# Performance work log

Measured on AMD Instinct MI355X. Metric: run time of the kernel, lower is better.

Reference implementation:

```python
import jax, jax.numpy as jnp
import numpy as np

N = 100000
E = 2000000
F = 64          # in_features == out_features (required by attention * h_j)
BETA = 0.5
NEG_SLOPE = 0.01  # torch F.leaky_relu default


def setup_inputs() -> dict:
    key = jax.random.key(0)
    k1, k2, k3, k4, k5, k6 = jax.random.split(key, 6)
    h = jax.random.normal(k1, (N, F), dtype=jnp.float32)
    adj = jax.random.randint(k2, (2, E), 0, N, dtype=jnp.int64)
    amount = jax.random.uniform(k3, (E,), dtype=jnp.float32)
    count = jax.random.uniform(k4, (E,), dtype=jnp.float32)
    fc_w = jax.random.normal(k5, (F, 2 * F), dtype=jnp.float32) * (1.0 / np.sqrt(2 * F))
    fc_b = jax.random.normal(k6, (F,), dtype=jnp.float32) * 0.01
    return {"h": h, "adj": adj, "amount": amount, "count": count,
            "fc_w": fc_w, "fc_b": fc_b}


def _minmax_norm(x):
    lo, hi = x.min(), x.max()
    return (x - lo) / (hi - lo + 1e-8)


def reference(h, adj, amount, count, fc_w, fc_b):
    # per-edge weight from normalized amount/count
    edge_weight = BETA * _minmax_norm(amount) + (1.0 - BETA) * _minmax_norm(count)  # [E]

    src, dst = adj[0], adj[1]
    h_i = h[src]                     # [E, F]
    h_j = h[dst]                     # [E, F]
    h_cat = jnp.concatenate([h_i, h_j], axis=1)  # [E, 2F]

    score = jnp.einsum('ef,of->eo', h_cat, fc_w) + fc_b  # [E, F_out]
    score = jnp.where(score >= 0, score, NEG_SLOPE * score)  # leaky_relu
    score = score * edge_weight[:, None]

    # softmax over ALL edges (dim 0), per feature, as in the original
    attention = jax.nn.softmax(score, axis=0)  # [E, F]

    agg = jnp.zeros_like(h).at[src].add(attention * h_j)  # scatter-add -> [N, F]
    return agg
```

## Files before the change

### kernel.cpp

```cpp
#include <hip/hip_runtime.h>
#include <hip/hip_fp16.h>
#include <math.h>

#define FDIM   64
#define NB     64
#define BSHIFT 9
#define BMASK  511
#define EPTA   16
#define CHUNKA (EPTA * 256)
#define SCH    1024
#define DMASK  0xFFFFF

__global__ __launch_bounds__(256) void count_mm_k(const int* __restrict__ src,
                                                  const float* __restrict__ amount,
                                                  const float* __restrict__ count,
                                                  int* __restrict__ mat,
                                                  float4* __restrict__ partial,
                                                  double* __restrict__ colsum,
                                                  int E, int nblkA, int nbkt) {
  __shared__ int lhist[512];
  __shared__ float4 lred[4];
  for (int k = threadIdx.x; k < nbkt; k += 256) lhist[k] = 0;
  if (blockIdx.x == 0)
    for (int i = threadIdx.x; i < 1024; i += 256) colsum[i] = 0.0;
  __syncthreads();
  float amin = 3.4e38f, amax = -3.4e38f, cmin = 3.4e38f, cmax = -3.4e38f;
  int e0 = blockIdx.x * CHUNKA + threadIdx.x * EPTA;
  if (e0 + EPTA <= E) {
    #pragma unroll
    for (int q = 0; q < EPTA; q += 4) {
      int4   s4 = *(const int4*)(src + e0 + q);
      float4 a4 = *(const float4*)(amount + e0 + q);
      float4 c4 = *(const float4*)(count + e0 + q);
      atomicAdd(&lhist[s4.x >> BSHIFT], 1);
      atomicAdd(&lhist[s4.y >> BSHIFT], 1);
      atomicAdd(&lhist[s4.z >> BSHIFT], 1);
      atomicAdd(&lhist[s4.w >> BSHIFT], 1);
      amin = fminf(amin, fminf(fminf(a4.x, a4.y), fminf(a4.z, a4.w)));
      amax = fmaxf(amax, fmaxf(fmaxf(a4.x, a4.y), fmaxf(a4.z, a4.w)));
      cmin = fminf(cmin, fminf(fminf(c4.x, c4.y), fminf(c4.z, c4.w)));
      cmax = fmaxf(cmax, fmaxf(fmaxf(c4.x, c4.y), fmaxf(c4.z, c4.w)));
    }
  } else {
    for (int e = e0; e < E; e++) {
      atomicAdd(&lhist[src[e] >> BSHIFT], 1);
      float a = amount[e], c = count[e];
      amin = fminf(amin, a); amax = fmaxf(amax, a);
      cmin = fminf(cmin, c); cmax = fmaxf(cmax, c);
    }
  }
  #pragma unroll
  for (int off = 32; off; off >>= 1) {
    amin = fminf(amin, __shfl_down(amin, off));
    amax = fmaxf(amax, __shfl_down(amax, off));
    cmin = fminf(cmin, __shfl_down(cmin, off));
    cmax = fmaxf(cmax, __shfl_down(cmax, off));
  }
  if ((threadIdx.x & 63) == 0) lred[threadIdx.x >> 6] = make_float4(amin, amax, cmin, cmax);
  __syncthreads();
  for (int k = threadIdx.x; k < nbkt; k += 256)
    mat[(size_t)k * nblkA + blockIdx.x] = lhist[k];
  if (threadIdx.x == 0) {
    float4 r = lred[0];
    #pragma unroll
    for (int w = 1; w < 4; w++) {
      r.x = fminf(r.x, lred[w].x); r.y = fmaxf(r.y, lred[w].y);
      r.z = fminf(r.z, lred[w].z); r.w = fmaxf(r.w, lred[w].w);
    }
    partial[blockIdx.x] = r;
  }
}

__global__ __launch_bounds__(256) void scan1_k(const int* __restrict__ v,
                                               int* __restrict__ bsum, int M) {
  __shared__ int lds[256];
  int t = threadIdx.x, b = blockIdx.x;
  int s = 0;
  for (int i = b * SCH + t; i < min((b + 1) * SCH, M); i += 256) s += v[i];
  lds[t] = s; __syncthreads();
  for (int off = 128; off; off >>= 1) {
    if (t < off) lds[t] += lds[t + off];
    __syncthreads();
  }
  if (t == 0) bsum[b] = lds[0];
}

__global__ __launch_bounds__(256) void scan2_k(const int* __restrict__ bsum,
                                               int* __restrict__ bexcl, int nchunk,
                                               const float4* __restrict__ partial,
                                               float* __restrict__ mmf, int nb) {
  __shared__ int lds[256];
  int t = threadIdx.x;
  int running = 0;
  for (int c0 = 0; c0 < nchunk; c0 += 256) {
    int x = (c0 + t < nchunk) ? bsum[c0 + t] : 0;
    lds[t] = x; __syncthreads();
    for (int off = 1; off < 256; off <<= 1) {
      int v = (t >= off) ? lds[t - off] : 0;
      __syncthreads();
      lds[t] += v; __syncthreads();
    }
    if (c0 + t < nchunk) bexcl[c0 + t] = running + lds[t] - x;
    running += lds[255];
    __syncthreads();
  }
  float amin = 3.4e38f, amax = -3.4e38f, cmin = 3.4e38f, cmax = -3.4e38f;
  for (int i = t; i < nb; i += 256) {
    float4 p = partial[i];
    amin = fminf(amin, p.x); amax = fmaxf(amax, p.y);
    cmin = fminf(cmin, p.z); cmax = fmaxf(cmax, p.w);
  }
  #pragma unroll
  for (int off = 32; off; off >>= 1) {
    amin = fminf(amin, __shfl_down(amin, off));
    amax = fmaxf(amax, __shfl_down(amax, off));
    cmin = fminf(cmin, __shfl_down(cmin, off));
    cmax = fmaxf(cmax, __shfl_down(cmax, off));
  }
  __shared__ float4 lred[4];
  if ((t & 63) == 0) lred[t >> 6] = make_float4(amin, amax, cmin, cmax);
  __syncthreads();
  if (t == 0) {
    float4 r = lred[0];
    #pragma unroll
    for (int w = 1; w < 4; w++) {
      r.x = fminf(r.x, lred[w].x); r.y = fmaxf(r.y, lred[w].y);
      r.z = fminf(r.z, lred[w].z); r.w = fmaxf(r.w, lred[w].w);
    }
    mmf[0] = r.x; mmf[1] = r.y; mmf[2] = r.z; mmf[3] = r.w;
  }
}

__global__ __launch_bounds__(256) void scan3_k(const int* __restrict__ v,
                                               const int* __restrict__ bexcl,
                                               int* __restrict__ smat, int M) {
  __shared__ int lds[256];
  int t = threadIdx.x, b = blockIdx.x;
  int running = bexcl[b];
  for (int tile = 0; tile < SCH; tile += 256) {
    int i = b * SCH + tile + t;
    int x = (i < M) ? v[i] : 0;
    lds[t] = x; __syncthreads();
    for (int off = 1; off < 256; off <<= 1) {
      int vv = (t >= off) ? lds[t - off] : 0;
      __syncthreads();
      lds[t] += vv; __syncthreads();
    }
    if (i < M) smat[i] = running + lds[t] - x;
    running += lds[255];
    __syncthreads();
  }
}

__global__ __launch_bounds__(256) void scatter_k(const int* __restrict__ src,
                                                 const int* __restrict__ dst,
                                                 const float* __restrict__ amount,
                                                 const float* __restrict__ count,
                                                 const float* __restrict__ mmf,
                                                 const int* __restrict__ smat,
                                                 int2* __restrict__ payload,
                                                 int E, int nblkA, int nbkt) {
  __shared__ int cntb[512];
  __shared__ int baseb[512];
  __shared__ int sbase[512];
  __shared__ int wsum[4];
  __shared__ int2 lpay[CHUNKA];
  __shared__ int lgpos[CHUNKA];
  const int t = threadIdx.x, blk = blockIdx.x;
  for (int k = t; k < nbkt; k += 256) {
    cntb[k] = 0;
    sbase[k] = smat[(size_t)k * nblkA + blk];
  }
  __syncthreads();
  const float amin = mmf[0], amax = mmf[1], cmin = mmf[2], cmax = mmf[3];
  const float L2E = 1.4426950408889634f;
  const float ascale = 0.5f * L2E / (amax - amin + 1e-8f);
  const float cscale = 0.5f * L2E / (cmax - cmin + 1e-8f);
  int e0 = blk * CHUNKA + t * EPTA;
  const bool full = (e0 + EPTA <= E);
  int4 S[4]; int4 D[4]; float4 A[4]; float4 C[4];
  if (full) {
    #pragma unroll
    for (int q = 0; q < 4; q++) {
      S[q] = *(const int4*)(src + e0 + 4 * q);
      D[q] = *(const int4*)(dst + e0 + 4 * q);
      A[q] = *(const float4*)(amount + e0 + 4 * q);
      C[q] = *(const float4*)(count + e0 + 4 * q);
      atomicAdd(&cntb[S[q].x >> BSHIFT], 1);
      atomicAdd(&cntb[S[q].y >> BSHIFT], 1);
      atomicAdd(&cntb[S[q].z >> BSHIFT], 1);
      atomicAdd(&cntb[S[q].w >> BSHIFT], 1);
    }
  } else {
    for (int e = e0; e < E; e++) atomicAdd(&cntb[src[e] >> BSHIFT], 1);
  }
  __syncthreads();
  {
    const int wv = t >> 6, ln = t & 63;
    int carry = 0;
    #pragma unroll
    for (int c = 0; c < 4; c++) {
      int idx = (wv << 8) + (c << 6) + ln;
      int x = (idx < nbkt) ? cntb[idx] : 0;
      int v = x;
      #pragma unroll
      for (int off = 1; off < 64; off <<= 1) {
        int u = __shfl_up(v, off);
        if (ln >= off) v += u;
      }
      if (idx < nbkt) baseb[idx] = carry + v - x;
      carry += __shfl(v, 63);
    }
    if (ln == 0) wsum[wv] = carry;
  }
  __syncthreads();
  {
    const int wv = t >> 6, ln = t & 63;
    int wpre = 0;
    #pragma unroll
    for (int i = 0; i < 4; i++) wpre += (i < wv) ? wsum[i] : 0;
    if (wpre) {
      #pragma unroll
      for (int c = 0; c < 4; c++) {
        int idx = (wv << 8) + (c << 6) + ln;
        if (idx < nbkt) baseb[idx] += wpre;
      }
    }
  }
  __syncthreads();
  for (int k = t; k < nbkt; k += 256) cntb[k] = baseb[k];
  __syncthreads();
  auto ins = [&](int s, int d, float a, float c) {
    int b = s >> BSHIFT;
    float ew = (a - amin) * ascale + (c - cmin) * cscale;
    int pos = atomicAdd(&cntb[b], 1);
    lpay[pos] = make_int2(d | ((s & BMASK) << 20), __float_as_int(ew));
    lgpos[pos] = sbase[b] + (pos - baseb[b]);
  };
  if (full) {
    #pragma unroll
    for (int q = 0; q < 4; q++) {
      ins(S[q].x, D[q].x, A[q].x, C[q].x);
      ins(S[q].y, D[q].y, A[q].y, C[q].y);
      ins(S[q].z, D[q].z, A[q].z, C[q].z);
      ins(S[q].w, D[q].w, A[q].w, C[q].w);
    }
  } else {
    for (int e = e0; e < E; e++) ins(src[e], dst[e], amount[e], count[e]);
  }
  __syncthreads();
  const int ned = min(CHUNKA, E - blk * CHUNKA);
  for (int i = t; i < ned; i += 256) payload[lgpos[i]] = lpay[i];
}

__global__ __launch_bounds__(256) void binB_k(const int2* __restrict__ payload,
                                              const int* __restrict__ smat,
                                              int2* __restrict__ edge_s,
                                              int E, int nblkA, int nbkt) {
  __shared__ int fcnt[512];
  __shared__ int fbase[512];
  __shared__ int tmp[256];
  const int b = blockIdx.x;
  const int t = threadIdx.x;
  const int base = smat[(size_t)b * nblkA];
  const int end  = (b + 1 < nbkt) ? smat[(size_t)(b + 1) * nblkA] : E;
  fcnt[t] = 0; fcnt[t + 256] = 0;
  __syncthreads();
  for (int i = base + t; i < end; i += 256)
    atomicAdd(&fcnt[payload[i].x >> 20], 1);
  __syncthreads();
  int running = 0;
  for (int c0 = 0; c0 < 512; c0 += 256) {
    int x = fcnt[c0 + t];
    tmp[t] = x; __syncthreads();
    for (int off = 1; off < 256; off <<= 1) {
      int v = (t >= off) ? tmp[t - off] : 0;
      __syncthreads();
      tmp[t] += v; __syncthreads();
    }
    fbase[c0 + t] = running + tmp[t] - x;
    running += tmp[255];
    __syncthreads();
  }
  fcnt[t] = base + fbase[t];
  fcnt[t + 256] = base + fbase[t + 256];
  __syncthreads();
  for (int i = base + t; i < end; i += 256) {
    int2 v = payload[i];
    int pos = atomicAdd(&fcnt[v.x >> 20], 1);
    edge_s[pos] = v;
  }
}

__global__ __launch_bounds__(128) void pre_gemm(const float* __restrict__ h,
                                                const float* __restrict__ fc_w,
                                                const float* __restrict__ fc_b,
                                                float* __restrict__ G1,
                                                __half2* __restrict__ P, int N) {
  __shared__ float hs[NB * FDIM];
  const int t = threadIdx.x;
  const int o = t & 63, half = t >> 6;
  float w[FDIM];
  const float* wrow = fc_w + o * 128 + half * 64;
  #pragma unroll
  for (int f = 0; f < FDIM; f += 4) {
    float4 v = *(const float4*)(wrow + f);
    w[f] = v.x; w[f + 1] = v.y; w[f + 2] = v.z; w[f + 3] = v.w;
  }
  const float bias = (half == 0) ? fc_b[o] : 0.0f;
  const int n0 = blockIdx.x * NB;
  const int nrows = min(NB, N - n0);
  {
    const float4* hsrc = (const float4*)(h + (size_t)n0 * FDIM);
    float4* hd = (float4*)hs;
    for (int i = t; i < nrows * (FDIM / 4); i += 128) hd[i] = hsrc[i];
  }
  __syncthreads();
  for (int n = 0; n < nrows; n++) {
    float acc = bias;
    #pragma unroll
    for (int f = 0; f < FDIM; f += 4) {
      float4 hv = *(const float4*)(&hs[n * FDIM + f]);
      acc += hv.x * w[f] + hv.y * w[f + 1] + hv.z * w[f + 2] + hv.w * w[f + 3];
    }
    if (half == 0) {
      G1[(size_t)(n0 + n) * FDIM + o] = acc;
    } else {
      P[(size_t)(n0 + n) * FDIM + o] =
          __halves2half2(__float2half(acc), __float2half(hs[n * FDIM + o]));
    }
  }
}

__device__ __forceinline__ float2 unpack_h2(unsigned u) {
  __half2 v = *(__half2*)&u;
  return make_float2(__low2float(v), __high2float(v));
}

__global__ __launch_bounds__(256) void fused_k(const int2* __restrict__ edge_s,
                                               const int* __restrict__ smat,
                                               const float* __restrict__ G1,
                                               const unsigned* __restrict__ P,
                                               double* __restrict__ colsum,
                                               float* __restrict__ out,
                                               int E, int nblkA, int nbkt) {
  const int lane = threadIdx.x & 63;
  const int wv = __builtin_amdgcn_readfirstlane(threadIdx.x >> 6);
  const int wid = blockIdx.x * 4 + wv;
  const int nw = gridDim.x * 4;
  float csum = 0.0f;
  const int per = (((E + nw - 1) / nw) + 63) & ~63;
  const int e0 = wid * per;
  const int e1 = min(e0 + per, E);
  if (e0 < E) {
    int lo = 0, hi = nbkt - 1;
    while (lo < hi) {
      int mid = (lo + hi + 1) >> 1;
      if (smat[(size_t)mid * nblkA] <= e0) lo = mid; else hi = mid - 1;
    }
    int bkt = lo;
    int nextb = (bkt + 1 < nbkt) ? smat[(size_t)(bkt + 1) * nblkA] : E;
    int curnode = -1;
    bool firstf = true;
    float acc = 0.0f, g1 = 0.0f;
    auto flush_to = [&](int node) {
      if (curnode >= 0) {
        float* dp = out + (size_t)curnode * FDIM + lane;
        if (firstf) { atomicAdd(dp, acc); firstf = false; }
        else *dp = acc;
      }
      curnode = node; acc = 0.0f;
      g1 = G1[(size_t)node * FDIM + lane];
    };
    for (int c0 = e0; c0 < e1; c0 += 64) {
      const int m = min(64, e1 - c0);
      int2 p = make_int2(0, 0);
      if (lane < m) p = edge_s[c0 + lane];
      if (m == 64) {
        #pragma unroll 1
        for (int j = 0; j < 64; j += 16) {
          int dd[16], nd[16]; float ee[16]; unsigned uu[16];
          #pragma unroll
          for (int k = 0; k < 16; k++) {
            int x = __builtin_amdgcn_readlane(p.x, j + k);
            ee[k] = __int_as_float(__builtin_amdgcn_readlane(p.y, j + k));
            dd[k] = x & DMASK;
            nd[k] = x >> 20;
          }
          #pragma unroll
          for (int k = 0; k < 16; k++) uu[k] = P[(size_t)dd[k] * FDIM + lane];
          #pragma unroll
          for (int k = 0; k < 16; k++) {
            int i = c0 + j + k;
            while (i >= nextb) { bkt++; nextb = (bkt + 1 < nbkt) ? smat[(size_t)(bkt + 1) * nblkA] : E; }
            int node = (bkt << BSHIFT) + nd[k];
            if (node != curnode) flush_to(node);
            float2 v = unpack_h2(uu[k]);
            float sc = g1 + v.x;
            sc = fmaxf(sc, 0.01f * sc);
            float x = exp2f(sc * ee[k]);
            csum += x;
            acc += x * v.y;
          }
        }
      } else {
        for (int j = 0; j < m; j += 16) {
          const int rem = m - j;
          int dd[16], nd[16]; float ee[16]; unsigned uu[16];
          #pragma unroll
          for (int k = 0; k < 16; k++) {
            int x = __builtin_amdgcn_readlane(p.x, j + k);
            ee[k] = __int_as_float(__builtin_amdgcn_readlane(p.y, j + k));
            dd[k] = x & DMASK;
            nd[k] = x >> 20;
          }
          #pragma unroll
          for (int k = 0; k < 16; k++) uu[k] = P[(size_t)dd[k] * FDIM + lane];
          #pragma unroll
          for (int k = 0; k < 16; k++) {
            if (k < rem) {
              int i = c0 + j + k;
              while (i >= nextb) { bkt++; nextb = (bkt + 1 < nbkt) ? smat[(size_t)(bkt + 1) * nblkA] : E; }
              int node = (bkt << BSHIFT) + nd[k];
              if (node != curnode) flush_to(node);
              float2 v = unpack_h2(uu[k]);
              float sc = g1 + v.x;
              sc = fmaxf(sc, 0.01f * sc);
              float x = exp2f(sc * ee[k]);
              csum += x;
              acc += x * v.y;
            }
          }
        }
      }
    }
    if (curnode >= 0) atomicAdd(out + (size_t)curnode * FDIM + lane, acc);
  }
  __shared__ float part[256];
  part[threadIdx.x] = csum;
  __syncthreads();
  if (threadIdx.x < 64) {
    float tot = part[threadIdx.x] + part[threadIdx.x + 64] +
                part[threadIdx.x + 128] + part[threadIdx.x + 192];
    atomicAdd(&colsum[threadIdx.x * 16], (double)tot);
  }
}

__global__ __launch_bounds__(256) void scale_k(float4* __restrict__ out4,
                                               const double* __restrict__ colsum,
                                               int total4) {
  __shared__ float rinv_s[64];
  if (threadIdx.x < 64) rinv_s[threadIdx.x] = (float)(1.0 / colsum[threadIdx.x * 16]);
  __syncthreads();
  const float4* r4 = (const float4*)rinv_s;
  int idx = blockIdx.x * blockDim.x + threadIdx.x;
  int stride = gridDim.x * blockDim.x;
  for (int i = idx; i < total4; i += stride) {
    float4 v = out4[i];
    float4 r = r4[i & 15];
    v.x *= r.x; v.y *= r.y; v.z *= r.z; v.w *= r.w;
    out4[i] = v;
  }
}

extern "C" void kernel_launch(void* const* d_in, const int* in_sizes, int n_in,
                              void* d_out, int out_size, void* d_ws, size_t ws_size,
                              hipStream_t stream) {
  const float* h      = (const float*)d_in[0];
  const int*   adj    = (const int*)d_in[1];
  const float* amount = (const float*)d_in[2];
  const float* count  = (const float*)d_in[3];
  const float* fc_w   = (const float*)d_in[4];
  const float* fc_b   = (const float*)d_in[5];
  float* out = (float*)d_out;

  const int E = in_sizes[2];
  const int N = in_sizes[0] / FDIM;
  const int* src = adj;
  const int* dst = adj + E;
  const int nbkt  = (N + BMASK) >> BSHIFT;
  const int nblkA = (E + CHUNKA - 1) / CHUNKA;
  const int M = nbkt * nblkA;
  const int nchunk = (M + SCH - 1) / SCH;

  char* ws = (char*)d_ws;
  size_t off = 0;
  auto alloc = [&](size_t bytes) { void* p = ws + off; off += (bytes + 255) & ~(size_t)255; return p; };
  float*    G1      = (float*)alloc((size_t)N * FDIM * sizeof(float));
  __half2*  P       = (__half2*)alloc((size_t)N * FDIM * sizeof(__half2));
  int2*     edge_s  = (int2*)alloc((size_t)E * sizeof(int2));
  int2*     payload = (int2*)alloc((size_t)E * sizeof(int2));
  int*      mat     = (int*)alloc((size_t)M * sizeof(int));
  int*      smat    = (int*)alloc((size_t)M * sizeof(int));
  int*      bsum    = (int*)alloc((size_t)nchunk * sizeof(int));
  int*      bexcl   = (int*)alloc((size_t)nchunk * sizeof(int));
  float4*   mmpart  = (float4*)alloc((size_t)nblkA * sizeof(float4));
  double*   colsum  = (double*)alloc(1024 * sizeof(double));
  float*    mmf     = (float*)alloc(4 * sizeof(float));

  hipMemsetAsync(d_out, 0, (size_t)out_size * sizeof(float), stream);
  count_mm_k<<<nblkA, 256, 0, stream>>>(src, amount, count, mat, mmpart, colsum, E, nblkA, nbkt);
  scan1_k<<<nchunk, 256, 0, stream>>>(mat, bsum, M);
  scan2_k<<<1, 256, 0, stream>>>(bsum, bexcl, nchunk, mmpart, mmf, nblkA);
  scan3_k<<<nchunk, 256, 0, stream>>>(mat, bexcl, smat, M);
  scatter_k<<<nblkA, 256, 0, stream>>>(src, dst, amount, count, mmf, smat, payload, E, nblkA, nbkt);
  binB_k<<<nbkt, 256, 0, stream>>>(payload, smat, edge_s, E, nblkA, nbkt);
  pre_gemm<<<(N + NB - 1) / NB, 128, 0, stream>>>(h, fc_w, fc_b, G1, P, N);
  fused_k<<<4096, 256, 0, stream>>>(edge_s, smat, G1, (const unsigned*)P, colsum, out, E, nblkA, nbkt);
  scale_k<<<1024, 256, 0, stream>>>((float4*)out, colsum, N * FDIM / 4);
}
```

Baseline: 307.2 us.

## Replace per-block histogram matrix scans with global atomic bucket cursors

Measured after the change: 314.2 us. 2.3% more time.

```diff
diff --git a/kernel.cpp b/kernel.cpp
--- a/kernel.cpp
+++ b/kernel.cpp
@@ -3,26 +3,23 @@
 #include <math.h>
 
 #define FDIM   64
-#define NB     64
-#define BSHIFT 9
-#define BMASK  511
+#define NB     128
+#define BSHIFT 8
+#define BMASK  255
 #define EPTA   16
 #define CHUNKA (EPTA * 256)
-#define SCH    1024
 #define DMASK  0xFFFFF
+#define MAXBKT 512
 
 __global__ __launch_bounds__(256) void count_mm_k(const int* __restrict__ src,
                                                   const float* __restrict__ amount,
                                                   const float* __restrict__ count,
-                                                  int* __restrict__ mat,
+                                                  int* __restrict__ bktTotal,
                                                   float4* __restrict__ partial,
-                                                  double* __restrict__ colsum,
-                                                  int E, int nblkA, int nbkt) {
-  __shared__ int lhist[512];
+                                                  int E, int nbkt) {
+  __shared__ int lhist[MAXBKT];
   __shared__ float4 lred[4];
   for (int k = threadIdx.x; k < nbkt; k += 256) lhist[k] = 0;
-  if (blockIdx.x == 0)
-    for (int i = threadIdx.x; i < 1024; i += 256) colsum[i] = 0.0;
   __syncthreads();
   float amin = 3.4e38f, amax = -3.4e38f, cmin = 3.4e38f, cmax = -3.4e38f;
   int e0 = blockIdx.x * CHUNKA + threadIdx.x * EPTA;
@@ -59,7 +56,7 @@
   if ((threadIdx.x & 63) == 0) lred[threadIdx.x >> 6] = make_float4(amin, amax, cmin, cmax);
   __syncthreads();
   for (int k = threadIdx.x; k < nbkt; k += 256)
-    mat[(size_t)k * nblkA + blockIdx.x] = lhist[k];
+    if (lhist[k]) atomicAdd(&bktTotal[k], lhist[k]);
   if (threadIdx.x == 0) {
     float4 r = lred[0];
     #pragma unroll
@@ -71,39 +68,35 @@
   }
 }
 
-__global__ __launch_bounds__(256) void scan1_k(const int* __restrict__ v,
-                                               int* __restrict__ bsum, int M) {
-  __shared__ int lds[256];
-  int t = threadIdx.x, b = blockIdx.x;
-  int s = 0;
-  for (int i = b * SCH + t; i < min((b + 1) * SCH, M); i += 256) s += v[i];
-  lds[t] = s; __syncthreads();
-  for (int off = 128; off; off >>= 1) {
-    if (t < off) lds[t] += lds[t + off];
+__global__ __launch_bounds__(256) void scanB_k(const int* __restrict__ bktTotal,
+                                               int* __restrict__ bbase,
+                                               int* __restrict__ cursor,
+                                               const float4* __restrict__ partial,
+                                               float* __restrict__ mmf,
+                                               int nbkt, int nb, int E) {
+  __shared__ int lds[MAXBKT];
+  const int t = threadIdx.x;
+  for (int k = t; k < nbkt; k += 256) lds[k] = bktTotal[k];
+  __syncthreads();
+  __shared__ int tmp[256];
+  int running = 0;
+  for (int c0 = 0; c0 < nbkt; c0 += 256) {
+    int x = (c0 + t < nbkt) ? lds[c0 + t] : 0;
+    tmp[t] = x; __syncthreads();
+    for (int off = 1; off < 256; off <<= 1) {
+      int v = (t >= off) ? tmp[t - off] : 0;
+      __syncthreads();
+      tmp[t] += v; __syncthreads();
+    }
+    if (c0 + t < nbkt) {
+      int b = running + tmp[t] - x;
+      bbase[c0 + t] = b;
+      cursor[c0 + t] = b;
+    }
+    running += tmp[255];
     __syncthreads();
   }
-  if (t == 0) bsum[b] = lds[0];
-}
-
-__global__ __launch_bounds__(256) void scan2_k(const int* __restrict__ bsum,
-                                               int* __restrict__ bexcl, int nchunk,
-                                               const float4* __restrict__ partial,
-                                               float* __restrict__ mmf, int nb) {
-  __shared__ int lds[256];
-  int t = threadIdx.x;
-  int running = 0;
-  for (int c0 = 0; c0 < nchunk; c0 += 256) {
-    int x = (c0 + t < nchunk) ? bsum[c0 + t] : 0;
-    lds[t] = x; __syncthreads();
-    for (int off = 1; off < 256; off <<= 1) {
-      int v = (t >= off) ? lds[t - off] : 0;
-      __syncthreads();
-      lds[t] += v; __syncthreads();
-    }
-    if (c0 + t < nchunk) bexcl[c0 + t] = running + lds[t] - x;
-    running += lds[255];
-    __syncthreads();
-  }
+  if (t == 0) bbase[nbkt] = E;
   float amin = 3.4e38f, amax = -3.4e38f, cmin = 3.4e38f, cmax = -3.4e38f;
   for (int i = t; i < nb; i += 256) {
     float4 p = partial[i];
@@ -131,52 +124,24 @@
   }
 }
 
-__global__ __launch_bounds__(256) void scan3_k(const int* __restrict__ v,
-                                               const int* __restrict__ bexcl,
-                                               int* __restrict__ smat, int M) {
-  __shared__ int lds[256];
-  int t = threadIdx.x, b = blockIdx.x;
-  int running = bexcl[b];
-  for (int tile = 0; tile < SCH; tile += 256) {
-    int i = b * SCH + tile + t;
-    int x = (i < M) ? v[i] : 0;
-    lds[t] = x; __syncthreads();
-    for (int off = 1; off < 256; off <<= 1) {
-      int vv = (t >= off) ? lds[t - off] : 0;
-      __syncthreads();
-      lds[t] += vv; __syncthreads();
-    }
-    if (i < M) smat[i] = running + lds[t] - x;
-    running += lds[255];
-    __syncthreads();
-  }
-}
-
 __global__ __launch_bounds__(256) void scatter_k(const int* __restrict__ src,
                                                  const int* __restrict__ dst,
                                                  const float* __restrict__ amount,
                                                  const float* __restrict__ count,
                                                  const float* __restrict__ mmf,
-                                                 const int* __restrict__ smat,
+                                                 int* __restrict__ cursor,
                                                  int2* __restrict__ payload,
-                                                 int E, int nblkA, int nbkt) {
-  __shared__ int cntb[512];
-  __shared__ int baseb[512];
-  __shared__ int sbase[512];
-  __shared__ int wsum[4];
-  __shared__ int2 lpay[CHUNKA];
-  __shared__ int lgpos[CHUNKA];
-  const int t = threadIdx.x, blk = blockIdx.x;
-  for (int k = t; k < nbkt; k += 256) {
-    cntb[k] = 0;
-    sbase[k] = smat[(size_t)k * nblkA + blk];
-  }
+                                                 int E, int nbkt) {
+  __shared__ int lhist[MAXBKT];
+  __shared__ int lcur[MAXBKT];
+  const int t = threadIdx.x;
+  for (int k = t; k < nbkt; k += 256) lhist[k] = 0;
   __syncthreads();
   const float amin = mmf[0], amax = mmf[1], cmin = mmf[2], cmax = mmf[3];
   const float L2E = 1.4426950408889634f;
   const float ascale = 0.5f * L2E / (amax - amin + 1e-8f);
   const float cscale = 0.5f * L2E / (cmax - cmin + 1e-8f);
-  int e0 = blk * CHUNKA + t * EPTA;
+  int e0 = blockIdx.x * CHUNKA + t * EPTA;
   const bool full = (e0 + EPTA <= E);
   int4 S[4]; int4 D[4]; float4 A[4]; float4 C[4];
   if (full) {
@@ -186,56 +151,23 @@
       D[q] = *(const int4*)(dst + e0 + 4 * q);
       A[q] = *(const float4*)(amount + e0 + 4 * q);
       C[q] = *(const float4*)(count + e0 + 4 * q);
-      atomicAdd(&cntb[S[q].x >> BSHIFT], 1);
-      atomicAdd(&cntb[S[q].y >> BSHIFT], 1);
-      atomicAdd(&cntb[S[q].z >> BSHIFT], 1);
-      atomicAdd(&cntb[S[q].w >> BSHIFT], 1);
+      atomicAdd(&lhist[S[q].x >> BSHIFT], 1);
+      atomicAdd(&lhist[S[q].y >> BSHIFT], 1);
+      atomicAdd(&lhist[S[q].z >> BSHIFT], 1);
+      atomicAdd(&lhist[S[q].w >> BSHIFT], 1);
     }
   } else {
-    for (int e = e0; e < E; e++) atomicAdd(&cntb[src[e] >> BSHIFT], 1);
-  }
-  __syncthreads();
-  {
-    const int wv = t >> 6, ln = t & 63;
-    int carry = 0;
-    #pragma unroll
-    for (int c = 0; c < 4; c++) {
-      int idx = (wv << 8) + (c << 6) + ln;
-      int x = (idx < nbkt) ? cntb[idx] : 0;
-      int v = x;
-      #pragma unroll
-      for (int off = 1; off < 64; off <<= 1) {
-        int u = __shfl_up(v, off);
-        if (ln >= off) v += u;
-      }
-      if (idx < nbkt) baseb[idx] = carry + v - x;
-      carry += __shfl(v, 63);
-    }
-    if (ln == 0) wsum[wv] = carry;
-  }
-  __syncthreads();
-  {
-    const int wv = t >> 6, ln = t & 63;
-    int wpre = 0;
-    #pragma unroll
-    for (int i = 0; i < 4; i++) wpre += (i < wv) ? wsum[i] : 0;
-    if (wpre) {
-      #pragma unroll
-      for (int c = 0; c < 4; c++) {
-        int idx = (wv << 8) + (c << 6) + ln;
-        if (idx < nbkt) baseb[idx] += wpre;
-      }
-    }
-  }
-  __syncthreads();
-  for (int k = t; k < nbkt; k += 256) cntb[k] = baseb[k];
+    for (int e = e0; e < E; e++) atomicAdd(&lhist[src[e] >> BSHIFT], 1);
+  }
+  __syncthreads();
+  for (int k = t; k < nbkt; k += 256)
+    lcur[k] = lhist[k] ? atomicAdd(&cursor[k], lhist[k]) : 0;
   __syncthreads();
   auto ins = [&](int s, int d, float a, float c) {
     int b = s >> BSHIFT;
     float ew = (a - amin) * ascale + (c - cmin) * cscale;
-    int pos = atomicAdd(&cntb[b], 1);
-    lpay[pos] = make_int2(d | ((s & BMASK) << 20), __float_as_int(ew));
-    lgpos[pos] = sbase[b] + (pos - baseb[b]);
+    int pos = atomicAdd(&lcur[b], 1);
+    payload[pos] = make_int2(d | ((s & BMASK) << 20), __float_as_int(ew));
   };
   if (full) {
     #pragma unroll
@@ -248,58 +180,48 @@
   } else {
     for (int e = e0; e < E; e++) ins(src[e], dst[e], amount[e], count[e]);
   }
-  __syncthreads();
-  const int ned = min(CHUNKA, E - blk * CHUNKA);
-  for (int i = t; i < ned; i += 256) payload[lgpos[i]] = lpay[i];
 }
 
 __global__ __launch_bounds__(256) void binB_k(const int2* __restrict__ payload,
-                                              const int* __restrict__ smat,
+                                              const int* __restrict__ bbase,
                                               int2* __restrict__ edge_s,
-                                              int E, int nblkA, int nbkt) {
-  __shared__ int fcnt[512];
-  __shared__ int fbase[512];
+                                              int E, int nbkt) {
+  __shared__ int fcnt[256];
   __shared__ int tmp[256];
+  __shared__ int fcur[256];
   const int b = blockIdx.x;
   const int t = threadIdx.x;
-  const int base = smat[(size_t)b * nblkA];
-  const int end  = (b + 1 < nbkt) ? smat[(size_t)(b + 1) * nblkA] : E;
-  fcnt[t] = 0; fcnt[t + 256] = 0;
+  const int base = bbase[b];
+  const int end  = bbase[b + 1];
+  fcnt[t] = 0;
   __syncthreads();
   for (int i = base + t; i < end; i += 256)
-    atomicAdd(&fcnt[payload[i].x >> 20], 1);
-  __syncthreads();
-  int running = 0;
-  for (int c0 = 0; c0 < 512; c0 += 256) {
-    int x = fcnt[c0 + t];
-    tmp[t] = x; __syncthreads();
-    for (int off = 1; off < 256; off <<= 1) {
-      int v = (t >= off) ? tmp[t - off] : 0;
-      __syncthreads();
-      tmp[t] += v; __syncthreads();
-    }
-    fbase[c0 + t] = running + tmp[t] - x;
-    running += tmp[255];
+    atomicAdd(&fcnt[(payload[i].x >> 20) & BMASK], 1);
+  __syncthreads();
+  int x = fcnt[t];
+  tmp[t] = x; __syncthreads();
+  for (int off = 1; off < 256; off <<= 1) {
+    int v = (t >= off) ? tmp[t - off] : 0;
     __syncthreads();
-  }
-  fcnt[t] = base + fbase[t];
-  fcnt[t + 256] = base + fbase[t + 256];
+    tmp[t] += v; __syncthreads();
+  }
+  fcur[t] = base + tmp[t] - x;
   __syncthreads();
   for (int i = base + t; i < end; i += 256) {
     int2 v = payload[i];
-    int pos = atomicAdd(&fcnt[v.x >> 20], 1);
+    int pos = atomicAdd(&fcur[(v.x >> 20) & BMASK], 1);
     edge_s[pos] = v;
   }
 }
 
-__global__ __launch_bounds__(128) void pre_gemm(const float* __restrict__ h,
+__global__ __launch_bounds__(256) void pre_gemm(const float* __restrict__ h,
                                                 const float* __restrict__ fc_w,
                                                 const float* __restrict__ fc_b,
                                                 float* __restrict__ G1,
                                                 __half2* __restrict__ P, int N) {
   __shared__ float hs[NB * FDIM];
   const int t = threadIdx.x;
-  const int o = t & 63, half = t >> 6;
+  const int o = t & 63, half = (t >> 6) & 1, rg = t >> 7;
   float w[FDIM];
   const float* wrow = fc_w + o * 128 + half * 64;
   #pragma unroll
@@ -313,10 +235,12 @@
   {
     const float4* hsrc = (const float4*)(h + (size_t)n0 * FDIM);
     float4* hd = (float4*)hs;
-    for (int i = t; i < nrows * (FDIM / 4); i += 128) hd[i] = hsrc[i];
-  }
-  __syncthreads();
-  for (int n = 0; n < nrows; n++) {
+    for (int i = t; i < nrows * (FDIM / 4); i += 256) hd[i] = hsrc[i];
+  }
+  __syncthreads();
+  const int r0 = rg * 64;
+  const int r1 = min(r0 + 64, nrows);
+  for (int n = r0; n < r1; n++) {
     float acc = bias;
     #pragma unroll
     for (int f = 0; f < FDIM; f += 4) {
@@ -338,12 +262,12 @@
 }
 
 __global__ __launch_bounds__(256) void fused_k(const int2* __restrict__ edge_s,
-                                               const int* __restrict__ smat,
+                                               const int* __restrict__ bbase,
                                                const float* __restrict__ G1,
                                                const unsigned* __restrict__ P,
                                                double* __restrict__ colsum,
                                                float* __restrict__ out,
-                                               int E, int nblkA, int nbkt) {
+                                               int E, int nbkt) {
   const int lane = threadIdx.x & 63;
   const int wv = __builtin_amdgcn_readfirstlane(threadIdx.x >> 6);
   const int wid = blockIdx.x * 4 + wv;
@@ -356,10 +280,10 @@
     int lo = 0, hi = nbkt - 1;
     while (lo < hi) {
       int mid = (lo + hi + 1) >> 1;
-      if (smat[(size_t)mid * nblkA] <= e0) lo = mid; else hi = mid - 1;
+      if (bbase[mid] <= e0) lo = mid; else hi = mid - 1;
     }
     int bkt = lo;
-    int nextb = (bkt + 1 < nbkt) ? smat[(size_t)(bkt + 1) * nblkA] : E;
+    int nextb = bbase[bkt + 1];
     int curnode = -1;
     bool firstf = true;
     float acc = 0.0f, g1 = 0.0f;
@@ -385,14 +309,14 @@
             int x = __builtin_amdgcn_readlane(p.x, j + k);
             ee[k] = __int_as_float(__builtin_amdgcn_readlane(p.y, j + k));
             dd[k] = x & DMASK;
-            nd[k] = x >> 20;
+            nd[k] = (x >> 20) & BMASK;
           }
           #pragma unroll
           for (int k = 0; k < 16; k++) uu[k] = P[(size_t)dd[k] * FDIM + lane];
           #pragma unroll
           for (int k = 0; k < 16; k++) {
             int i = c0 + j + k;
-            while (i >= nextb) { bkt++; nextb = (bkt + 1 < nbkt) ? smat[(size_t)(bkt + 1) * nblkA] : E; }
+            while (i >= nextb) { bkt++; nextb = bbase[bkt + 1]; }
             int node = (bkt << BSHIFT) + nd[k];
             if (node != curnode) flush_to(node);
             float2 v = unpack_h2(uu[k]);
@@ -412,7 +336,7 @@
             int x = __builtin_amdgcn_readlane(p.x, j + k);
             ee[k] = __int_as_float(__builtin_amdgcn_readlane(p.y, j + k));
             dd[k] = x & DMASK;
-            nd[k] = x >> 20;
+            nd[k] = (x >> 20) & BMASK;
           }
           #pragma unroll
           for (int k = 0; k < 16; k++) uu[k] = P[(size_t)dd[k] * FDIM + lane];
@@ -420,7 +344,7 @@
           for (int k = 0; k < 16; k++) {
             if (k < rem) {
               int i = c0 + j + k;
-              while (i >= nextb) { bkt++; nextb = (bkt + 1 < nbkt) ? smat[(size_t)(bkt + 1) * nblkA] : E; }
+              while (i >= nextb) { bkt++; nextb = bbase[bkt + 1]; }
               int node = (bkt << BSHIFT) + nd[k];
               if (node != curnode) flush_to(node);
               float2 v = unpack_h2(uu[k]);
@@ -480,32 +404,29 @@
   const int* dst = adj + E;
   const int nbkt  = (N + BMASK) >> BSHIFT;
   const int nblkA = (E + CHUNKA - 1) / CHUNKA;
-  const int M = nbkt * nblkA;
-  const int nchunk = (M + SCH - 1) / SCH;
 
   char* ws = (char*)d_ws;
   size_t off = 0;
   auto alloc = [&](size_t bytes) { void* p = ws + off; off += (bytes + 255) & ~(size_t)255; return p; };
-  float*    G1      = (float*)alloc((size_t)N * FDIM * sizeof(float));
-  __half2*  P       = (__half2*)alloc((size_t)N * FDIM * sizeof(__half2));
-  int2*     edge_s  = (int2*)alloc((size_t)E * sizeof(int2));
-  int2*     payload = (int2*)alloc((size_t)E * sizeof(int2));
-  int*      mat     = (int*)alloc((size_t)M * sizeof(int));
-  int*      smat    = (int*)alloc((size_t)M * sizeof(int));
-  int*      bsum    = (int*)alloc((size_t)nchunk * sizeof(int));
-  int*      bexcl   = (int*)alloc((size_t)nchunk * sizeof(int));
-  float4*   mmpart  = (float4*)alloc((size_t)nblkA * sizeof(float4));
-  double*   colsum  = (double*)alloc(1024 * sizeof(double));
-  float*    mmf     = (float*)alloc(4 * sizeof(float));
+  float*    G1       = (float*)alloc((size_t)N * FDIM * sizeof(float));
+  __half2*  P        = (__half2*)alloc((size_t)N * FDIM * sizeof(__half2));
+  int2*     edge_s   = (int2*)alloc((size_t)E * sizeof(int2));
+  int2*     payload  = (int2*)alloc((size_t)E * sizeof(int2));
+  char*     ctrl     = (char*)alloc(MAXBKT * sizeof(int) + 1024 * sizeof(double));
+  int*      bktTotal = (int*)ctrl;
+  double*   colsum   = (double*)(ctrl + MAXBKT * sizeof(int));
+  int*      bbase    = (int*)alloc((MAXBKT + 1) * sizeof(int));
+  int*      cursor   = (int*)alloc(MAXBKT * sizeof(int));
+  float4*   mmpart   = (float4*)alloc((size_t)nblkA * sizeof(float4));
+  float*    mmf      = (float*)alloc(4 * sizeof(float));
 
   hipMemsetAsync(d_out, 0, (size_t)out_size * sizeof(float), stream);
-  count_mm_k<<<nblkA, 256, 0, stream>>>(src, amount, count, mat, mmpart, colsum, E, nblkA, nbkt);
-  scan1_k<<<nchunk, 256, 0, stream>>>(mat, bsum, M);
-  scan2_k<<<1, 256, 0, stream>>>(bsum, bexcl, nchunk, mmpart, mmf, nblkA);
-  scan3_k<<<nchunk, 256, 0, stream>>>(mat, bexcl, smat, M);
-  scatter_k<<<nblkA, 256, 0, stream>>>(src, dst, amount, count, mmf, smat, payload, E, nblkA, nbkt);
-  binB_k<<<nbkt, 256, 0, stream>>>(payload, smat, edge_s, E, nblkA, nbkt);
-  pre_gemm<<<(N + NB - 1) / NB, 128, 0, stream>>>(h, fc_w, fc_b, G1, P, N);
-  fused_k<<<4096, 256, 0, stream>>>(edge_s, smat, G1, (const unsigned*)P, colsum, out, E, nblkA, nbkt);
+  hipMemsetAsync(ctrl, 0, MAXBKT * sizeof(int) + 1024 * sizeof(double), stream);
+  count_mm_k<<<nblkA, 256, 0, stream>>>(src, amount, count, bktTotal, mmpart, E, nbkt);
+  scanB_k<<<1, 256, 0, stream>>>(bktTotal, bbase, cursor, mmpart, mmf, nbkt, nblkA, E);
+  scatter_k<<<nblkA, 256, 0, stream>>>(src, dst, amount, count, mmf, cursor, payload, E, nbkt);
+  binB_k<<<nbkt, 256, 0, stream>>>(payload, bbase, edge_s, E, nbkt);
+  pre_gemm<<<(N + NB - 1) / NB, 256, 0, stream>>>(h, fc_w, fc_b, G1, P, N);
+  fused_k<<<4096, 256, 0, stream>>>(edge_s, bbase, G1, (const unsigned*)P, colsum, out, E, nbkt);
   scale_k<<<1024, 256, 0, stream>>>((float4*)out, colsum, N * FDIM / 4);
 }
```
